# Optimization experiments

Hardware: AMD Instinct MI355X
Metric: run time of the kernel (lower is better)

The kernel has to match this reference:

```python
import jax, jax.numpy as jnp
import numpy as np


def _cal_similarity(query, respond):
    # query: [B, n1, d], respond: [B, n2, d]
    # scores[b, c, q, r] = <query[b, q], respond[c, r]>
    scores = jnp.einsum('bqd,crd->bcqr', query, respond)  # [B, B, n1, n2]
    # max over respond tokens, mean over query tokens -> [B, B]
    return scores.max(axis=-1).mean(axis=-1)


def _ce_with_arange_labels(logits):
    # cross-entropy with labels = arange(B), mean reduction
    logp = jax.nn.log_softmax(logits, axis=-1)
    return -jnp.mean(jnp.diagonal(logp))


def setup_inputs() -> dict:
    key = jax.random.key(0)
    k1, k2 = jax.random.split(key)
    B, n1, n2, d = 96, 196, 77, 512
    image_out = jax.random.normal(k1, (B, n1, d), dtype=jnp.float32)
    text_out = jax.random.normal(k2, (B, n2, d), dtype=jnp.float32)
    return {"image_out": image_out, "text_out": text_out}


def reference(image_out, text_out):
    i2t = _cal_similarity(image_out, text_out)  # [B, B]
    t2i = _cal_similarity(text_out, image_out)  # [B, B]
    return 0.5 * (_ce_with_arange_labels(i2t) + _ce_with_arange_labels(t2i))
```

## Files before the change

### kernel.cpp

```cpp
#include <hip/hip_runtime.h>
#include <math.h>

#define BB 96
#define N1 196
#define N2 77
#define DD 512

#define IMGN (BB * N1 * DD)
#define TXTN (BB * N2 * DD)

#define ATILES 13
#define NTILES 13
#define BUFH (NTILES * 512)

#define TA_TILES (BB * 13 * 16)
#define TB_TILES (BB * 5 * 16)
#define NT_TILES (TA_TILES + TB_TILES)

#define NSTRIPS_A (BB * 13)
#define NSTRIPS_B (BB * 5)
#define NSTRIPS   (NSTRIPS_A + NSTRIPS_B)

typedef _Float16 f16x8 __attribute__((ext_vector_type(8)));
typedef float f4v __attribute__((ext_vector_type(4)));

typedef unsigned int __attribute__((address_space(1))) as1_uint;
typedef unsigned int __attribute__((address_space(3))) as3_uint;

__device__ __forceinline__ void gload_lds16(const void* g, void* l) {
    __builtin_amdgcn_global_load_lds((const as1_uint*)g, (as3_uint*)l, 16, 0, 0);
}

__global__ __launch_bounds__(256) void convert_tiled_kernel(
    const float* __restrict__ img, const float* __restrict__ txt,
    _Float16* __restrict__ dst)
{
    __shared__ _Float16 sh[16 * 520];
    const int sid = blockIdx.x;
    const int tid = threadIdx.x;
    const float* base;
    int rowbase, rmax, tile0;
    if (sid < NSTRIPS_A) {
        const int bi = sid / 13, s = sid % 13;
        base = img + (size_t)bi * N1 * DD;
        rowbase = s * 16; rmax = N1 - 1;
        tile0 = sid * 16;
    } else {
        const int bs = sid - NSTRIPS_A;
        const int bt = bs / 5, ct = bs % 5;
        base = txt + (size_t)bt * N2 * DD;
        rowbase = ct * 16; rmax = N2 - 1;
        tile0 = TA_TILES + bs * 16;
    }
#pragma unroll
    for (int it = 0; it < 8; ++it) {
        const int u  = it * 256 + tid;
        const int r  = u >> 7;
        const int c4 = u & 127;
        int q = rowbase + r; q = q > rmax ? rmax : q;
        float4 v = *(const float4*)(base + (size_t)q * DD + c4 * 4);
        union { _Float16 h[4]; uint2 u2; } o;
        o.h[0] = (_Float16)v.x; o.h[1] = (_Float16)v.y;
        o.h[2] = (_Float16)v.z; o.h[3] = (_Float16)v.w;
        *(uint2*)(sh + r * 520 + c4 * 4) = o.u2;
    }
    __syncthreads();
#pragma unroll
    for (int it = 0; it < 4; ++it) {
        const int w  = it * 256 + tid;
        const int kc = w >> 6;
        const int c  = w & 63;
        const int r16 = c & 15, k8 = c >> 4;
        uint4 val = *(const uint4*)(sh + r16 * 520 + kc * 32 + k8 * 8);
        *(uint4*)(dst + (size_t)(tile0 + kc) * 512 + c * 8) = val;
    }
}

template <int SG0, int NS>
__device__ __forceinline__ void compute_sub(const f16x8* __restrict__ fr,
                                            const f16x8* __restrict__ b,
                                            f4v* __restrict__ acc, int lane) {
#pragma unroll
    for (int i = 0; i < NS; ++i) {
        f16x8 a = fr[(SG0 + i) * 64 + lane];
#pragma unroll
        for (int ct = 0; ct < 5; ++ct)
            acc[i * 5 + ct] = __builtin_amdgcn_mfma_f32_16x16x32_f16(
                a, b[ct], acc[i * 5 + ct], 0, 0, 0);
    }
}

template <int SG0, int NS, int H>
__device__ __forceinline__ void reduce_phase1(const f4v* __restrict__ acc,
                                              int g, int lq, int lm,
                                              float* __restrict__ rp,
                                              float* __restrict__ cp) {
    float colm[5];
#pragma unroll
    for (int ct = 0; ct < 5; ++ct) colm[ct] = -INFINITY;
#pragma unroll
    for (int i = 0; i < NS; ++i) {
        const int s = SG0 + i;
        float rowm[4] = {-INFINITY, -INFINITY, -INFINITY, -INFINITY};
        bool rows_ok = (s != 12) || (lq == 0);
#pragma unroll
        for (int ct = 0; ct < 5; ++ct) {
            f4v a = acc[i * 5 + ct];
            bool col_ok = (ct != 4) || (lm < N2 - 64);
            float cm = fmaxf(fmaxf(a[0], a[1]), fmaxf(a[2], a[3]));
            colm[ct] = fmaxf(colm[ct], rows_ok ? cm : -INFINITY);
#pragma unroll
            for (int r = 0; r < 4; ++r)
                rowm[r] = fmaxf(rowm[r], col_ok ? a[r] : -INFINITY);
        }
#pragma unroll
        for (int r = 0; r < 4; ++r) {
            float m = rowm[r];
            m = fmaxf(m, __shfl_xor(m, 1));
            m = fmaxf(m, __shfl_xor(m, 2));
            m = fmaxf(m, __shfl_xor(m, 4));
            m = fmaxf(m, __shfl_xor(m, 8));
            if (lm == 0) rp[H * 208 + s * 16 + lq * 4 + r] = m;
        }
    }
#pragma unroll
    for (int ct = 0; ct < 5; ++ct) {
        float m = colm[ct];
        m = fmaxf(m, __shfl_xor(m, 16));
        m = fmaxf(m, __shfl_xor(m, 32));
        if (lq == 0) cp[g * 160 + H * 80 + ct * 16 + lm] = m;
    }
}

template <bool PRE>
__global__ __launch_bounds__(512, 4) void sim_mfma_kernel(
    const float* __restrict__ imgF, const float* __restrict__ txtF,
    const _Float16* __restrict__ h16,
    float* __restrict__ i2t, float* __restrict__ t2i)
{
    const int id  = blockIdx.x;
    const int xcd = id & 7;
    const int lid = id >> 3;
    const int w   = lid % 48;
    const int btq = lid / 48;
    const int btp = btq * 4 + (w & 3);
    const int bi  = xcd * 12 + (w >> 2);
    const int bt0 = btp * 2;

    const int tid = threadIdx.x;
    const int wave = tid >> 6, lane = tid & 63;
    const int lm = lane & 15;
    const int lq = lane >> 4;
    const int g = wave >> 1;
    const int h = wave & 1;

    __shared__ __align__(16) _Float16 lds[3 * BUFH];
    float* rp   = (float*)lds;
    float* cp   = (float*)lds + 416;
    float* sws  = (float*)lds + 1056;
    float* scol = (float*)lds + 1064;

    int offA0 = 0, offA1 = 0;
    const float* fA0; const float* fA1;
    if constexpr (PRE) {
        offA0 = ((bi * 13 + wave) * 16) * 512 + lane * 8;
        if (wave < 5) offA1 = ((bi * 13 + 8 + wave) * 16) * 512 + lane * 8;
    } else {
        int q0 = wave * 16 + lm; q0 = q0 > (N1 - 1) ? (N1 - 1) : q0;
        offA0 = (bi * N1 + q0) * DD + lq * 8;
        fA0 = imgF;
        int q1 = (8 + wave) * 16 + lm; q1 = q1 > (N1 - 1) ? (N1 - 1) : q1;
        offA1 = (bi * N1 + q1) * DD + lq * 8;
        fA1 = imgF;
    }

    const f16x8* gb = nullptr;
    if constexpr (PRE)
        gb = (const f16x8*)h16 + (TA_TILES + (bt0 + h) * 5 * 16) * 64 + lane;

    auto stage = [&](int kc, int b) {
        const int k0 = kc * 512;
        gload_lds16(h16 + offA0 + k0, lds + (b * NTILES + wave) * 512);
        if (wave < 5)
            gload_lds16(h16 + offA1 + k0, lds + (b * NTILES + 8 + wave) * 512);
    };

    f4v acc[20];
#pragma unroll
    for (int i = 0; i < 20; ++i) acc[i] = (f4v){0.f, 0.f, 0.f, 0.f};

    auto do_compute = [&](const f16x8* fr, const f16x8* b) {
        if (wave == 0 || wave == 1)      compute_sub<0, 4>(fr, b, acc, lane);
        else if (wave == 2 || wave == 3) compute_sub<4, 3>(fr, b, acc, lane);
        else if (wave == 4 || wave == 5) compute_sub<7, 3>(fr, b, acc, lane);
        else                             compute_sub<10, 3>(fr, b, acc, lane);
    };

    if constexpr (PRE) {
        stage(0, 0);
        stage(1, 1);
#pragma unroll 1
        for (int kc = 0; kc < 16; ++kc) {
            f16x8 bfr[5];
#pragma unroll
            for (int ct = 0; ct < 5; ++ct)
                bfr[ct] = gb[ct * 1024 + kc * 64];
            if (kc + 2 < 16) stage(kc + 2, (kc + 2) % 3);
            if (wave < 5) asm volatile("s_waitcnt vmcnt(9)" ::: "memory");
            else          asm volatile("s_waitcnt vmcnt(7)" ::: "memory");
            __builtin_amdgcn_s_barrier();
            asm volatile("" ::: "memory");
            do_compute((const f16x8*)(lds + (kc % 3) * BUFH), bfr);
            asm volatile("" ::: "memory");
            __builtin_amdgcn_s_barrier();
        }
    } else {
        const int btf = bt0 + h;
#pragma unroll 1
        for (int kc = 0; kc < 16; ++kc) {
            __syncthreads();
            const int k0 = kc * 32;
#pragma unroll
            for (int j = 0; j < 2; ++j) {
                const int T = j * 8 + wave;
                if (j == 0 || wave < 5) {
                    const float* src = (j ? fA1 : fA0) + (j ? offA1 : offA0) + k0;
                    float4 v0 = *(const float4*)(src);
                    float4 v1 = *(const float4*)(src + 4);
                    union { f16x8 f; uint4 u; } o;
                    o.f[0] = (_Float16)v0.x; o.f[1] = (_Float16)v0.y;
                    o.f[2] = (_Float16)v0.z; o.f[3] = (_Float16)v0.w;
                    o.f[4] = (_Float16)v1.x; o.f[5] = (_Float16)v1.y;
                    o.f[6] = (_Float16)v1.z; o.f[7] = (_Float16)v1.w;
                    ((uint4*)lds)[T * 64 + lane] = o.u;
                }
            }
            __syncthreads();
            f16x8 bfr[5];
#pragma unroll
            for (int ct = 0; ct < 5; ++ct) {
                int r = ct * 16 + lm; r = r > (N2 - 1) ? (N2 - 1) : r;
                const float* src = txtF + (btf * N2 + r) * DD + k0 + lq * 8;
                float4 v0 = *(const float4*)(src);
                float4 v1 = *(const float4*)(src + 4);
                f16x8 f;
                f[0] = (_Float16)v0.x; f[1] = (_Float16)v0.y;
                f[2] = (_Float16)v0.z; f[3] = (_Float16)v0.w;
                f[4] = (_Float16)v1.x; f[5] = (_Float16)v1.y;
                f[6] = (_Float16)v1.z; f[7] = (_Float16)v1.w;
                bfr[ct] = f;
            }
            do_compute((const f16x8*)lds, bfr);
        }
        __syncthreads();
    }

    if (wave == 0)      reduce_phase1<0, 4, 0>(acc, g, lq, lm, rp, cp);
    else if (wave == 1) reduce_phase1<0, 4, 1>(acc, g, lq, lm, rp, cp);
    else if (wave == 2) reduce_phase1<4, 3, 0>(acc, g, lq, lm, rp, cp);
    else if (wave == 3) reduce_phase1<4, 3, 1>(acc, g, lq, lm, rp, cp);
    else if (wave == 4) reduce_phase1<7, 3, 0>(acc, g, lq, lm, rp, cp);
    else if (wave == 5) reduce_phase1<7, 3, 1>(acc, g, lq, lm, rp, cp);
    else if (wave == 6) reduce_phase1<10, 3, 0>(acc, g, lq, lm, rp, cp);
    else                reduce_phase1<10, 3, 1>(acc, g, lq, lm, rp, cp);
    __syncthreads();

    {
        const int half = tid >> 8;
        const int t = tid & 255;
        float v = (t < N1) ? rp[half * 208 + t] : 0.f;
        v += __shfl_xor(v, 1);  v += __shfl_xor(v, 2);  v += __shfl_xor(v, 4);
        v += __shfl_xor(v, 8);  v += __shfl_xor(v, 16); v += __shfl_xor(v, 32);
        if (lane == 0) sws[wave] = v;
    }
    if (tid < 160) {
        float m = fmaxf(fmaxf(cp[tid], cp[160 + tid]),
                        fmaxf(cp[320 + tid], cp[480 + tid]));
        scol[tid] = m;
    }
    __syncthreads();
    if (tid == 0)
        i2t[bi * BB + bt0] =
            (sws[0] + sws[1] + sws[2] + sws[3]) * (1.f / (float)N1);
    if (tid == 1)
        i2t[bi * BB + bt0 + 1] =
            (sws[4] + sws[5] + sws[6] + sws[7]) * (1.f / (float)N1);
    if (wave < 2) {
        const float* c = scol + wave * 80;
        float cv = c[lane] + ((lane < N2 - 64) ? c[64 + lane] : 0.f);
        cv += __shfl_xor(cv, 1);  cv += __shfl_xor(cv, 2);  cv += __shfl_xor(cv, 4);
        cv += __shfl_xor(cv, 8);  cv += __shfl_xor(cv, 16); cv += __shfl_xor(cv, 32);
        if (lane == 0)
            t2i[(bt0 + wave) * BB + bi] = cv * (1.f / (float)N2);
    }
}

__global__ __launch_bounds__(1024) void ce_kernel(
    const float* __restrict__ i2t, const float* __restrict__ t2i,
    float* __restrict__ out)
{
    const int tid = threadIdx.x;
    const int wave = tid >> 6;
    const int lane = tid & 63;

    float total = 0.f;
#pragma unroll 1
    for (int rr = 0; rr < 12; ++rr) {
        const int row = rr * 16 + wave;
        const float* M = (row < BB) ? i2t : t2i;
        const int b = (row < BB) ? row : row - BB;
        const float* r = M + b * BB;
        float a = r[lane];
        float c = (lane < BB - 64) ? r[64 + lane] : -INFINITY;
        float m = fmaxf(a, c);
        m = fmaxf(m, __shfl_xor(m, 1));  m = fmaxf(m, __shfl_xor(m, 2));
        m = fmaxf(m, __shfl_xor(m, 4));  m = fmaxf(m, __shfl_xor(m, 8));
        m = fmaxf(m, __shfl_xor(m, 16)); m = fmaxf(m, __shfl_xor(m, 32));
        float s = expf(a - m) + ((lane < BB - 64) ? expf(c - m) : 0.f);
        s += __shfl_xor(s, 1);  s += __shfl_xor(s, 2);  s += __shfl_xor(s, 4);
        s += __shfl_xor(s, 8);  s += __shfl_xor(s, 16); s += __shfl_xor(s, 32);
        total += r[b] - (m + logf(s));
    }
    __shared__ float sp[16];
    if (lane == 0) sp[wave] = total;
    __syncthreads();
    if (tid == 0) {
        float t = 0.f;
#pragma unroll
        for (int i = 0; i < 16; ++i) t += sp[i];
        out[0] = -t * (1.f / (float)(2 * BB));
    }
}

extern "C" void kernel_launch(void* const* d_in, const int* in_sizes, int n_in,
                              void* d_out, int out_size, void* d_ws, size_t ws_size,
                              hipStream_t stream) {
    const float* img = (const float*)d_in[0];
    const float* txt = (const float*)d_in[1];
    float* i2t = (float*)d_ws;
    float* t2i = i2t + BB * BB;

    const size_t conv_off = 2 * BB * BB * sizeof(float);
    const size_t need = conv_off + (size_t)NT_TILES * 512 * sizeof(_Float16);

    const int nblocks = BB * (BB / 2);
    if (ws_size >= need) {
        _Float16* h16 = (_Float16*)((char*)d_ws + conv_off);
        convert_tiled_kernel<<<NSTRIPS, 256, 0, stream>>>(img, txt, h16);
        sim_mfma_kernel<true><<<nblocks, 512, 0, stream>>>(img, txt, h16, i2t, t2i);
    } else {
        sim_mfma_kernel<false><<<nblocks, 512, 0, stream>>>(img, txt, nullptr, i2t, t2i);
    }
    ce_kernel<<<1, 1024, 0, stream>>>(i2t, t2i, (float*)d_out);
}
```

Baseline: 281.0 us.

## Stage text B tiles through LDS with async loads instead of direct global reads

The text operand fragments are now brought into LDS alongside the image tiles via the same triple-buffered global_load_lds pipeline, growing each stage buffer from 13 to 24 tiles. Each wave then reads its B fragments from LDS instead of issuing direct global loads every k-step. This is meant to hide B load latency behind the asynchronous pipeline rather than stalling on per-iteration global reads. In exchange it triples LDS use per block, which may reduce occupancy, and it adds a dummy 24th tile load per stage.

Result: no change. 285.7 us (+1.7%).

```diff
diff --git a/kernel.cpp b/kernel.cpp
--- a/kernel.cpp
+++ b/kernel.cpp
@@ -10,7 +10,7 @@
 #define TXTN (BB * N2 * DD)
 
 #define ATILES 13
-#define NTILES 13
+#define NTILES 24
 #define BUFH (NTILES * 512)
 
 #define TA_TILES (BB * 13 * 16)
@@ -76,10 +76,13 @@
     }
 }
 
-template <int SG0, int NS>
+template <int SG0, int NS, int H>
 __device__ __forceinline__ void compute_sub(const f16x8* __restrict__ fr,
-                                            const f16x8* __restrict__ b,
                                             f4v* __restrict__ acc, int lane) {
+    f16x8 b[5];
+#pragma unroll
+    for (int ct = 0; ct < 5; ++ct)
+        b[ct] = fr[(ATILES + H * 5 + ct) * 64 + lane];
 #pragma unroll
     for (int i = 0; i < NS; ++i) {
         f16x8 a = fr[(SG0 + i) * 64 + lane];
@@ -152,7 +155,6 @@
     const int lm = lane & 15;
     const int lq = lane >> 4;
     const int g = wave >> 1;
-    const int h = wave & 1;
 
     __shared__ __align__(16) _Float16 lds[3 * BUFH];
     float* rp   = (float*)lds;
@@ -160,40 +162,64 @@
     float* sws  = (float*)lds + 1056;
     float* scol = (float*)lds + 1064;
 
-    int offA0 = 0, offA1 = 0;
-    const float* fA0; const float* fA1;
-    if constexpr (PRE) {
-        offA0 = ((bi * 13 + wave) * 16) * 512 + lane * 8;
-        if (wave < 5) offA1 = ((bi * 13 + 8 + wave) * 16) * 512 + lane * 8;
-    } else {
-        int q0 = wave * 16 + lm; q0 = q0 > (N1 - 1) ? (N1 - 1) : q0;
-        offA0 = (bi * N1 + q0) * DD + lq * 8;
-        fA0 = imgF;
-        int q1 = (8 + wave) * 16 + lm; q1 = q1 > (N1 - 1) ? (N1 - 1) : q1;
-        offA1 = (bi * N1 + q1) * DD + lq * 8;
-        fA1 = imgF;
-    }
-
-    const f16x8* gb = nullptr;
-    if constexpr (PRE)
-        gb = (const f16x8*)h16 + (TA_TILES + (bt0 + h) * 5 * 16) * 64 + lane;
+    int off[3];
+    const float* fsrc[3];
+#pragma unroll
+    for (int j = 0; j < 3; ++j) {
+        const int T = 8 * j + wave;
+        if constexpr (PRE) {
+            int t;
+            if (T < ATILES) {
+                t = (bi * 13 + T) * 16;
+            } else if (T < 23) {
+                const int ct = T - ATILES;
+                const int bt = bt0 + (ct >= 5);
+                t = TA_TILES + (bt * 5 + (ct % 5)) * 16;
+            } else {
+                t = 0;
+            }
+            off[j] = t * 512 + lane * 8;
+        } else {
+            int o;
+            bool isA = true;
+            if (T < ATILES) {
+                int q = T * 16 + lm; q = q > (N1 - 1) ? (N1 - 1) : q;
+                o = (bi * N1 + q) * DD + lq * 8;
+            } else if (T < 23) {
+                isA = false;
+                int ct = T - ATILES;
+                int bt = bt0 + (ct >= 5);
+                int r = (ct % 5) * 16 + lm; r = r > (N2 - 1) ? (N2 - 1) : r;
+                o = (bt * N2 + r) * DD + lq * 8;
+            } else {
+                o = lq * 8;
+            }
+            off[j] = o;
+            fsrc[j] = isA ? imgF : txtF;
+        }
+    }
 
     auto stage = [&](int kc, int b) {
         const int k0 = kc * 512;
-        gload_lds16(h16 + offA0 + k0, lds + (b * NTILES + wave) * 512);
-        if (wave < 5)
-            gload_lds16(h16 + offA1 + k0, lds + (b * NTILES + 8 + wave) * 512);
+#pragma unroll
+        for (int j = 0; j < 3; ++j)
+            gload_lds16(h16 + off[j] + k0,
+                        lds + (b * NTILES + 8 * j + wave) * 512);
     };
 
     f4v acc[20];
 #pragma unroll
     for (int i = 0; i < 20; ++i) acc[i] = (f4v){0.f, 0.f, 0.f, 0.f};
 
-    auto do_compute = [&](const f16x8* fr, const f16x8* b) {
-        if (wave == 0 || wave == 1)      compute_sub<0, 4>(fr, b, acc, lane);
-        else if (wave == 2 || wave == 3) compute_sub<4, 3>(fr, b, acc, lane);
-        else if (wave == 4 || wave == 5) compute_sub<7, 3>(fr, b, acc, lane);
-        else                             compute_sub<10, 3>(fr, b, acc, lane);
+    auto do_compute = [&](const f16x8* fr) {
+        if (wave == 0)      compute_sub<0, 4, 0>(fr, acc, lane);
+        else if (wave == 1) compute_sub<0, 4, 1>(fr, acc, lane);
+        else if (wave == 2) compute_sub<4, 3, 0>(fr, acc, lane);
+        else if (wave == 3) compute_sub<4, 3, 1>(fr, acc, lane);
+        else if (wave == 4) compute_sub<7, 3, 0>(fr, acc, lane);
+        else if (wave == 5) compute_sub<7, 3, 1>(fr, acc, lane);
+        else if (wave == 6) compute_sub<10, 3, 0>(fr, acc, lane);
+        else                compute_sub<10, 3, 1>(fr, acc, lane);
     };
 
     if constexpr (PRE) {
@@ -201,32 +227,31 @@
         stage(1, 1);
 #pragma unroll 1
         for (int kc = 0; kc < 16; ++kc) {
-            f16x8 bfr[5];
-#pragma unroll
-            for (int ct = 0; ct < 5; ++ct)
-                bfr[ct] = gb[ct * 1024 + kc * 64];
-            if (kc + 2 < 16) stage(kc + 2, (kc + 2) % 3);
-            if (wave < 5) asm volatile("s_waitcnt vmcnt(9)" ::: "memory");
-            else          asm volatile("s_waitcnt vmcnt(7)" ::: "memory");
+            if (kc < 14) {
+                stage(kc + 2, (kc + 2) % 3);
+                asm volatile("s_waitcnt vmcnt(6)" ::: "memory");
+            } else if (kc == 14) {
+                asm volatile("s_waitcnt vmcnt(3)" ::: "memory");
+            } else {
+                asm volatile("s_waitcnt vmcnt(0)" ::: "memory");
+            }
             __builtin_amdgcn_s_barrier();
             asm volatile("" ::: "memory");
-            do_compute((const f16x8*)(lds + (kc % 3) * BUFH), bfr);
+            do_compute((const f16x8*)(lds + (kc % 3) * BUFH));
             asm volatile("" ::: "memory");
             __builtin_amdgcn_s_barrier();
         }
     } else {
-        const int btf = bt0 + h;
 #pragma unroll 1
         for (int kc = 0; kc < 16; ++kc) {
             __syncthreads();
             const int k0 = kc * 32;
 #pragma unroll
-            for (int j = 0; j < 2; ++j) {
-                const int T = j * 8 + wave;
-                if (j == 0 || wave < 5) {
-                    const float* src = (j ? fA1 : fA0) + (j ? offA1 : offA0) + k0;
-                    float4 v0 = *(const float4*)(src);
-                    float4 v1 = *(const float4*)(src + 4);
+            for (int j = 0; j < 3; ++j) {
+                const int T = 8 * j + wave;
+                if (T < 23) {
+                    float4 v0 = *(const float4*)(fsrc[j] + off[j] + k0);
+                    float4 v1 = *(const float4*)(fsrc[j] + off[j] + k0 + 4);
                     union { f16x8 f; uint4 u; } o;
                     o.f[0] = (_Float16)v0.x; o.f[1] = (_Float16)v0.y;
                     o.f[2] = (_Float16)v0.z; o.f[3] = (_Float16)v0.w;
@@ -236,21 +261,7 @@
                 }
             }
             __syncthreads();
-            f16x8 bfr[5];
-#pragma unroll
-            for (int ct = 0; ct < 5; ++ct) {
-                int r = ct * 16 + lm; r = r > (N2 - 1) ? (N2 - 1) : r;
-                const float* src = txtF + (btf * N2 + r) * DD + k0 + lq * 8;
-                float4 v0 = *(const float4*)(src);
-                float4 v1 = *(const float4*)(src + 4);
-                f16x8 f;
-                f[0] = (_Float16)v0.x; f[1] = (_Float16)v0.y;
-                f[2] = (_Float16)v0.z; f[3] = (_Float16)v0.w;
-                f[4] = (_Float16)v1.x; f[5] = (_Float16)v1.y;
-                f[6] = (_Float16)v1.z; f[7] = (_Float16)v1.w;
-                bfr[ct] = f;
-            }
-            do_compute((const f16x8*)lds, bfr);
+            do_compute((const f16x8*)lds);
         }
         __syncthreads();
     }
```
